# Kernel optimization log

Hardware: AMD Instinct MI355X
Metric: run time of the kernel (lower is better)

The kernel has to match this reference:

```python
import jax, jax.numpy as jnp
import numpy as np

B, S, H, D = 4, 4096, 32, 64
STEP = 32
N_STEPS = S // STEP  # 128 rows in the step tables


def _make_step_tables():
    inv_freq = 1.0 / (10000.0 ** (np.arange(0, D, 2, dtype=np.float32) / D))
    t = np.arange(N_STEPS, dtype=np.float32) * STEP
    freqs = np.outer(t, inv_freq)               # [N_STEPS, D//2]
    emb = np.concatenate([freqs, freqs], axis=-1)  # [N_STEPS, D]
    return jnp.asarray(np.cos(emb), jnp.float32), jnp.asarray(np.sin(emb), jnp.float32)


def setup_inputs() -> dict:
    key = jax.random.key(0)
    k1, k2, k3 = jax.random.split(key, 3)
    cos_step, sin_step = _make_step_tables()
    return {
        "q": jax.random.normal(k1, (B, S, H, D), jnp.float32),
        "k": jax.random.normal(k2, (B, S, H, D), jnp.float32),
        "v": jax.random.normal(k3, (B, S, H, D), jnp.float32),
        "cos_step": cos_step,
        "sin_step": sin_step,
        "offset": 0,
    }


def _rotate_half(x):
    x1, x2 = jnp.split(x, 2, axis=-1)
    return jnp.concatenate([-x2, x1], axis=-1)


def _apply_rope(x, cos, sin):
    # cos/sin: [b, n, h, 1] broadcast over head_dim (faithful to gather-on-col-0)
    return x * cos + _rotate_half(x) * sin


def _contextual_positions(q, k):
    # q, k: [b, n, h, d] -> [b, h, n, d]
    qh = jnp.transpose(q, (0, 2, 1, 3))
    kh = jnp.transpose(k, (0, 2, 1, 3))
    qr = jax.nn.relu(qh)
    kr = jax.nn.relu(kh)
    qn = qr / (jnp.linalg.norm(qr, axis=-1, keepdims=True) + 1e-6)
    kn = kr / (jnp.linalg.norm(kr, axis=-1, keepdims=True) + 1e-6)
    # causal linear attention with v = ones: o_t = q_t . cumsum_{s<=t} k_s
    cumk = jnp.cumsum(kn, axis=2)                     # [b, h, n, d]
    pos = jnp.einsum('bhnd,bhnd->bhn', qn, cumk)      # identical across the 16 v dims
    pos = jnp.transpose(pos, (0, 2, 1))               # [b, n, h]
    return jnp.clip(pos / STEP, 0.0, float(N_STEPS - 1))


def reference(q, k, v, cos_step, sin_step, offset):
    pos = _contextual_positions(q, k)                 # [b, n, h], float in [0, N_STEPS-1]
    pf = jnp.floor(pos)
    pc = jnp.ceil(pos)
    pfi = pf.astype(jnp.int32)
    pci = pc.astype(jnp.int32)
    # torch.gather with index [..., 1] on the repeated table reads only column 0
    cos0 = cos_step[:, 0]
    sin0 = sin_step[:, 0]
    frac = pos - pf
    cosp = (cos0[pfi] + frac * (cos0[pci] - cos0[pfi]))[..., None]  # [b, n, h, 1]
    sinp = (sin0[pfi] + frac * (sin0[pci] - sin0[pfi]))[..., None]
    return _apply_rope(q, cosp, sinp), _apply_rope(k, cosp, sinp)
```

## Files before the change

### kernel.cpp

```cpp
#include <hip/hip_runtime.h>
#include <math.h>

#define BB 4
#define SS 4096
#define HH 32
#define DD 64
#define STEPF 32.0f
#define NSTEPS 128

#define SUBC 64
#define SC_PER_BH (SS / SUBC)
#define WAVES 4

__device__ __forceinline__ float wave_sum64(float v) {
    v += __shfl_xor(v, 1);
    v += __shfl_xor(v, 2);
    v += __shfl_xor(v, 4);
    v += __shfl_xor(v, 8);
    v += __shfl_xor(v, 16);
    v += __shfl_xor(v, 32);
    return v;
}

__global__ __launch_bounds__(256) void knorm_subchunk_sums(
    const float* __restrict__ k, float* __restrict__ sums) {
    const int lane = threadIdx.x & 63;
    const int wave = threadIdx.x >> 6;
    const int sc = blockIdx.x * WAVES + wave;
    const int h = blockIdx.y;
    const int b = blockIdx.z;
    const int p0 = sc * SUBC;
    size_t base = ((size_t)b * SS + p0) * (HH * DD) + (size_t)h * DD + lane;
    float acc = 0.f;
#pragma unroll 4
    for (int i = 0; i < SUBC; ++i) {
        float kv = k[base + (size_t)i * (HH * DD)];
        float kr = fmaxf(kv, 0.f);
        float ss = wave_sum64(kr * kr);
        float kn = kr / (sqrtf(ss) + 1e-6f);
        acc += kn;
    }
    sums[(((size_t)b * HH + h) * SC_PER_BH + sc) * DD + lane] = acc;
}

__global__ __launch_bounds__(256) void rope_apply(
    const float* __restrict__ q, const float* __restrict__ k,
    const float* __restrict__ cosst, const float* __restrict__ sinst,
    const float* __restrict__ sums,
    float* __restrict__ outq, float* __restrict__ outk) {
    const int lane = threadIdx.x & 63;
    const int wave = threadIdx.x >> 6;
    const int sc = blockIdx.x * WAVES + wave;
    const int h = blockIdx.y;
    const int b = blockIdx.z;

    const float* srow = sums + (((size_t)b * HH + h) * SC_PER_BH) * DD + lane;
    float off = 0.f;
    for (int cc = 0; cc < sc; ++cc) off += srow[(size_t)cc * DD];

    const int p0 = sc * SUBC;
    size_t base = ((size_t)b * SS + p0) * (HH * DD) + (size_t)h * DD + lane;
    float cumk = off;
#pragma unroll 4
    for (int i = 0; i < SUBC; ++i) {
        size_t idx = base + (size_t)i * (HH * DD);
        float kv = k[idx];
        float qv = q[idx];

        float kr = fmaxf(kv, 0.f);
        float kss = wave_sum64(kr * kr);
        float kn = kr / (sqrtf(kss) + 1e-6f);
        cumk += kn;

        float qr = fmaxf(qv, 0.f);
        float qss = wave_sum64(qr * qr);
        float qn = qr / (sqrtf(qss) + 1e-6f);

        float dot = wave_sum64(qn * cumk);
        float pos = dot * (1.0f / STEPF);
        pos = fminf(fmaxf(pos, 0.f), (float)(NSTEPS - 1));
        float pf = floorf(pos);
        int pfi = (int)pf;
        float frac = pos - pf;
        int pci = min(pfi + 1, NSTEPS - 1);

        float c0 = cosst[(size_t)pfi * DD];
        float c1 = cosst[(size_t)pci * DD];
        float s0 = sinst[(size_t)pfi * DD];
        float s1 = sinst[(size_t)pci * DD];
        float cosp = c0 + frac * (c1 - c0);
        float sinp = s0 + frac * (s1 - s0);

        float qo = __shfl_xor(qv, 32);
        float rq = (lane < 32) ? -qo : qo;
        float ko = __shfl_xor(kv, 32);
        float rk = (lane < 32) ? -ko : ko;

        outq[idx] = qv * cosp + rq * sinp;
        outk[idx] = kv * cosp + rk * sinp;
    }
}

extern "C" void kernel_launch(void* const* d_in, const int* in_sizes, int n_in,
                              void* d_out, int out_size, void* d_ws, size_t ws_size,
                              hipStream_t stream) {
    const float* q = (const float*)d_in[0];
    const float* k = (const float*)d_in[1];
    const float* cosst = (const float*)d_in[3];
    const float* sinst = (const float*)d_in[4];

    float* outq = (float*)d_out;
    float* outk = outq + (size_t)BB * SS * HH * DD;
    float* sums = (float*)d_ws;

    dim3 grid(SC_PER_BH / WAVES, HH, BB);
    knorm_subchunk_sums<<<grid, 256, 0, stream>>>(k, sums);
    rope_apply<<<grid, 256, 0, stream>>>(q, k, cosst, sinst, sums, outq, outk);
}
```

Measured before the change: 568.9 us.

## Precompute per-row norm reciprocals in phase one and use DPP reductions

Phase one now also reads q and computes the reciprocal norms of relu(q) and relu(k) for each row, folding the 1/STEP scale into the q factor. It stores them per position so phase two can drop two of its three wave reductions per row. Reductions switch to DPP/swizzle plus readlane, the cos/sin column-0 table with its deltas is staged in LDS, and the rotate-half uses ds_bpermute. The cost is an extra full read of q in phase one and extra workspace traffic. Using rcp instead of division may change rounding slightly.

Result: slower. 593.1 us (+4.2%).

```diff
diff --git a/kernel.cpp b/kernel.cpp
--- a/kernel.cpp
+++ b/kernel.cpp
@@ -5,25 +5,29 @@
 #define SS 4096
 #define HH 32
 #define DD 64
-#define STEPF 32.0f
 #define NSTEPS 128
 
 #define SUBC 64
 #define SC_PER_BH (SS / SUBC)
 #define WAVES 4
 
-__device__ __forceinline__ float wave_sum64(float v) {
-    v += __shfl_xor(v, 1);
-    v += __shfl_xor(v, 2);
-    v += __shfl_xor(v, 4);
-    v += __shfl_xor(v, 8);
-    v += __shfl_xor(v, 16);
-    v += __shfl_xor(v, 32);
-    return v;
+#define DPP_ADD(v, ctrl) \
+    ((v) + __int_as_float(__builtin_amdgcn_update_dpp(0, __float_as_int(v), (ctrl), 0xF, 0xF, true)))
+
+__device__ __forceinline__ float wave_allsum(float v) {
+    v = DPP_ADD(v, 0xB1);
+    v = DPP_ADD(v, 0x4E);
+    v = DPP_ADD(v, 0x141);
+    v = DPP_ADD(v, 0x140);
+    v = v + __int_as_float(__builtin_amdgcn_ds_swizzle(__float_as_int(v), 0x401F));
+    float a = __int_as_float(__builtin_amdgcn_readlane(__float_as_int(v), 0));
+    float b = __int_as_float(__builtin_amdgcn_readlane(__float_as_int(v), 32));
+    return a + b;
 }
 
-__global__ __launch_bounds__(256) void knorm_subchunk_sums(
-    const float* __restrict__ k, float* __restrict__ sums) {
+__global__ __launch_bounds__(256) void phase1(
+    const float* __restrict__ q, const float* __restrict__ k,
+    float* __restrict__ sums, float* __restrict__ krs_out, float* __restrict__ qrs_out) {
     const int lane = threadIdx.x & 63;
     const int wave = threadIdx.x >> 6;
     const int sc = blockIdx.x * WAVES + wave;
@@ -31,23 +35,50 @@
     const int b = blockIdx.z;
     const int p0 = sc * SUBC;
     size_t base = ((size_t)b * SS + p0) * (HH * DD) + (size_t)h * DD + lane;
+
     float acc = 0.f;
+    float krs_keep = 0.f, qrs_keep = 0.f;
 #pragma unroll 4
     for (int i = 0; i < SUBC; ++i) {
-        float kv = k[base + (size_t)i * (HH * DD)];
+        size_t idx = base + (size_t)i * (HH * DD);
+        float kv = k[idx];
+        float qv = q[idx];
         float kr = fmaxf(kv, 0.f);
-        float ss = wave_sum64(kr * kr);
-        float kn = kr / (sqrtf(ss) + 1e-6f);
-        acc += kn;
+        float qr = fmaxf(qv, 0.f);
+        float kss = wave_allsum(kr * kr);
+        float qss = wave_allsum(qr * qr);
+        float krs = __builtin_amdgcn_rcpf(sqrtf(kss) + 1e-6f);
+        float qrs = __builtin_amdgcn_rcpf((sqrtf(qss) + 1e-6f) * 32.0f);
+        acc += kr * krs;
+        krs_keep = (lane == i) ? krs : krs_keep;
+        qrs_keep = (lane == i) ? qrs : qrs_keep;
     }
     sums[(((size_t)b * HH + h) * SC_PER_BH + sc) * DD + lane] = acc;
+    size_t pbase = ((size_t)b * HH + h) * SS + (size_t)p0;
+    krs_out[pbase + lane] = krs_keep;
+    qrs_out[pbase + lane] = qrs_keep;
 }
 
-__global__ __launch_bounds__(256) void rope_apply(
+__global__ __launch_bounds__(256) void phase2(
     const float* __restrict__ q, const float* __restrict__ k,
     const float* __restrict__ cosst, const float* __restrict__ sinst,
     const float* __restrict__ sums,
+    const float* __restrict__ krs_in, const float* __restrict__ qrs_in,
     float* __restrict__ outq, float* __restrict__ outk) {
+    __shared__ float4 tbl[NSTEPS];
+    {
+        int t = threadIdx.x;
+        if (t < NSTEPS) {
+            int t1 = (t + 1 < NSTEPS) ? t + 1 : t;
+            float c0 = cosst[(size_t)t * DD];
+            float s0 = sinst[(size_t)t * DD];
+            float c1 = cosst[(size_t)t1 * DD];
+            float s1 = sinst[(size_t)t1 * DD];
+            tbl[t] = make_float4(c0, c1 - c0, s0, s1 - s0);
+        }
+    }
+    __syncthreads();
+
     const int lane = threadIdx.x & 63;
     const int wave = threadIdx.x >> 6;
     const int sc = blockIdx.x * WAVES + wave;
@@ -59,6 +90,13 @@
     for (int cc = 0; cc < sc; ++cc) off += srow[(size_t)cc * DD];
 
     const int p0 = sc * SUBC;
+    size_t pbase = ((size_t)b * HH + h) * SS + (size_t)p0;
+    float krs_vec = krs_in[pbase + lane];
+    float qrs_vec = qrs_in[pbase + lane];
+
+    const float sgn = (lane < 32) ? -1.f : 1.f;
+    const int xaddr = (lane ^ 32) << 2;
+
     size_t base = ((size_t)b * SS + p0) * (HH * DD) + (size_t)h * DD + lane;
     float cumk = off;
 #pragma unroll 4
@@ -67,37 +105,29 @@
         float kv = k[idx];
         float qv = q[idx];
 
-        float kr = fmaxf(kv, 0.f);
-        float kss = wave_sum64(kr * kr);
-        float kn = kr / (sqrtf(kss) + 1e-6f);
+        float krs = __int_as_float(__builtin_amdgcn_readlane(__float_as_int(krs_vec), i));
+        float qrs = __int_as_float(__builtin_amdgcn_readlane(__float_as_int(qrs_vec), i));
+
+        float kn = fmaxf(kv, 0.f) * krs;
         cumk += kn;
+        float qn = fmaxf(qv, 0.f) * qrs;
 
-        float qr = fmaxf(qv, 0.f);
-        float qss = wave_sum64(qr * qr);
-        float qn = qr / (sqrtf(qss) + 1e-6f);
-
-        float dot = wave_sum64(qn * cumk);
-        float pos = dot * (1.0f / STEPF);
+        float pos = wave_allsum(qn * cumk);
         pos = fminf(fmaxf(pos, 0.f), (float)(NSTEPS - 1));
         float pf = floorf(pos);
         int pfi = (int)pf;
         float frac = pos - pf;
-        int pci = min(pfi + 1, NSTEPS - 1);
 
-        float c0 = cosst[(size_t)pfi * DD];
-        float c1 = cosst[(size_t)pci * DD];
-        float s0 = sinst[(size_t)pfi * DD];
-        float s1 = sinst[(size_t)pci * DD];
-        float cosp = c0 + frac * (c1 - c0);
-        float sinp = s0 + frac * (s1 - s0);
+        float4 tv = tbl[pfi];
+        float cosp = fmaf(frac, tv.y, tv.x);
+        float sinp = fmaf(frac, tv.w, tv.z);
+        float rsin = sinp * sgn;
 
-        float qo = __shfl_xor(qv, 32);
-        float rq = (lane < 32) ? -qo : qo;
-        float ko = __shfl_xor(kv, 32);
-        float rk = (lane < 32) ? -ko : ko;
+        float rq = __int_as_float(__builtin_amdgcn_ds_bpermute(xaddr, __float_as_int(qv)));
+        float rk = __int_as_float(__builtin_amdgcn_ds_bpermute(xaddr, __float_as_int(kv)));
 
-        outq[idx] = qv * cosp + rq * sinp;
-        outk[idx] = kv * cosp + rk * sinp;
+        outq[idx] = fmaf(qv, cosp, rq * rsin);
+        outk[idx] = fmaf(kv, cosp, rk * rsin);
     }
 }
 
@@ -111,9 +141,12 @@
 
     float* outq = (float*)d_out;
     float* outk = outq + (size_t)BB * SS * HH * DD;
+
     float* sums = (float*)d_ws;
+    float* krs = sums + (size_t)BB * HH * SC_PER_BH * DD;
+    float* qrs = krs + (size_t)BB * HH * SS;
 
     dim3 grid(SC_PER_BH / WAVES, HH, BB);
-    knorm_subchunk_sums<<<grid, 256, 0, stream>>>(k, sums);
-    rope_apply<<<grid, 256, 0, stream>>>(q, k, cosst, sinst, sums, outq, outk);
+    phase1<<<grid, 256, 0, stream>>>(q, k, sums, krs, qrs);
+    phase2<<<grid, 256, 0, stream>>>(q, k, cosst, sinst, sums, krs, qrs, outq, outk);
 }
```
